# Optimization experiments

Hardware: AMD Instinct MI355X
Metric: run time of the kernel (lower is better)

## Reference

```python
import jax, jax.numpy as jnp
import numpy as np

B, N = 128, 65536
POS_FRAC = 0.02  # sparse positives, realistic for detection


def setup_inputs() -> dict:
    key = jax.random.key(0)
    k1, k2 = jax.random.split(key)
    pred = jax.random.normal(k1, (B, N), dtype=jnp.float32)
    label = (jax.random.uniform(k2, (B, N)) < POS_FRAC).astype(jnp.float32)
    return {"pred": pred, "label": label}


def _focal_loss_with_mask(pred, label, gamma=2.0, alpha=0.75, negative_ratio=3.0):
    # BCE with logits, elementwise: y*softplus(-x) + (1-y)*softplus(x)
    loss = label * jax.nn.softplus(-pred) + (1.0 - label) * jax.nn.softplus(pred)
    p = jax.nn.sigmoid(pred)
    p_t = label * p + (1.0 - label) * (1.0 - p)
    loss = loss * (1.0 - p_t) ** gamma
    loss = loss * (label * alpha + (1.0 - label) * (1.0 - alpha))

    fn_mask = (p < 0.5) & (label == 1.0)
    fp_mask = (p >= 0.5) & (label == 0.0)

    # --- hard negative mining (vectorized rank-based selection) ---
    pos_mask = label > 0
    num_pos = pos_mask.sum(axis=1, keepdims=True)              # [B,1]
    num_neg = jnp.floor(negative_ratio * num_pos).astype(jnp.int32)  # int() truncation as in torch
    loss_m = jnp.where(pos_mask, -jnp.inf, loss)               # positives sorted last
    order = jnp.argsort(-loss_m, axis=1)                       # descending sort indices
    ranks = jnp.argsort(order, axis=1)                         # rank of each element
    neg_mask = ranks < num_neg
    relevant = pos_mask | neg_mask

    w = alpha / (1.0 - alpha)
    loss = jnp.where(fn_mask | fp_mask, loss * w, loss)
    rm = relevant.astype(loss.dtype)
    return (loss * rm).sum() / rm.sum()


def reference(pred, label):
    return _focal_loss_with_mask(pred, label)
```

## Files before the change

kernel.cpp:

```cpp
#include <hip/hip_runtime.h>
#include <cstdint>
#include <cstddef>

constexpr int B_ROWS = 128;
constexpr int N_COLS = 65536;
constexpr int LIST_CAP = 8192;

constexpr size_t OFF_HISTCNT  = 0;
constexpr size_t OFF_HISTLOSS = (size_t)1 << 20;
constexpr size_t OFF_NUMPOS   = (size_t)2 << 20;
constexpr size_t OFF_SPOS     = ((size_t)2 << 20) + 512;
constexpr size_t OFF_ROWS     = ((size_t)2 << 20) + 1024;
constexpr size_t OFF_ROWDEN   = ((size_t)2 << 20) + 2048;
constexpr size_t ZERO_BYTES   = ((size_t)2 << 20) + 4096;
constexpr size_t OFF_KEYS     = (size_t)4 << 20;

__device__ __forceinline__ unsigned key_from_pred(float x) {
  unsigned b = __float_as_uint(x);
  return (b & 0x80000000u) ? ~b : (b | 0x80000000u);
}
__device__ __forceinline__ float pred_from_key(unsigned k) {
  unsigned b = (k & 0x80000000u) ? (k ^ 0x80000000u) : ~k;
  return __uint_as_float(b);
}

__device__ __forceinline__ float neg_loss(float x) {
  float ax = fabsf(x);
  float e  = expf(-ax);
  float p  = (x >= 0.0f) ? 1.0f / (1.0f + e) : e / (1.0f + e);
  float sp = fmaxf(x, 0.0f) + log1pf(e);
  float pt = 1.0f - p;
  float f  = 1.0f - pt;
  float l  = sp * f * f * 0.25f;
  return (p >= 0.5f) ? l * 3.0f : l;
}
__device__ __forceinline__ float pos_loss(float x) {
  float ax = fabsf(x);
  float e  = expf(-ax);
  float p  = (x >= 0.0f) ? 1.0f / (1.0f + e) : e / (1.0f + e);
  float sp = fmaxf(-x, 0.0f) + log1pf(e);
  float f  = 1.0f - p;
  float l  = sp * f * f * 0.75f;
  return (p < 0.5f) ? l * 3.0f : l;
}
__device__ __forceinline__ float loss_from_key(unsigned k) { return neg_loss(pred_from_key(k)); }

constexpr int K1_TPB = 256;
constexpr int K1_SEGS = 8;
constexpr int K1_SEG_ELEMS = N_COLS / K1_SEGS;
constexpr int K1_ITERS = K1_SEG_ELEMS / (K1_TPB * 4);

template <bool STORE_KEYS>
__global__ __launch_bounds__(K1_TPB)
void k1_hist(const float* __restrict__ pred, const float* __restrict__ label,
             int* __restrict__ histCnt, float* __restrict__ histLoss,
             int* __restrict__ numPos, float* __restrict__ SPos,
             unsigned* __restrict__ keys)
{
  __shared__ int   hcnt[2048];
  __shared__ float hloss[2048];
  __shared__ int   wnp[K1_TPB / 64];
  __shared__ float wsp[K1_TPB / 64];
  const int tid = threadIdx.x;
  for (int i = tid; i < 2048; i += K1_TPB) { hcnt[i] = 0; hloss[i] = 0.0f; }
  __syncthreads();

  const int row = blockIdx.x / K1_SEGS;
  const int seg = blockIdx.x % K1_SEGS;
  const size_t base = (size_t)row * N_COLS + (size_t)seg * K1_SEG_ELEMS;
  const float4* p4 = reinterpret_cast<const float4*>(pred + base);
  const float4* l4 = reinterpret_cast<const float4*>(label + base);
  uint4* k4 = STORE_KEYS ? reinterpret_cast<uint4*>(keys + base) : nullptr;

  int npos = 0; float spos = 0.0f;
  for (int it = 0; it < K1_ITERS; ++it) {
    const int vi = it * K1_TPB + tid;
    const float4 pv = p4[vi];
    const float4 lv = l4[vi];
    const float xs[4] = {pv.x, pv.y, pv.z, pv.w};
    const float ys[4] = {lv.x, lv.y, lv.z, lv.w};
    unsigned ks[4];
#pragma unroll
    for (int j = 0; j < 4; ++j) {
      const float x = xs[j];
      if (ys[j] > 0.5f) {
        npos += 1;
        spos += pos_loss(x);
        ks[j] = 0u;
      } else {
        const unsigned key = key_from_pred(x);
        ks[j] = key;
        atomicAdd(&hcnt[key >> 21], 1);
        atomicAdd(&hloss[key >> 21], neg_loss(x));
      }
    }
    if (STORE_KEYS) { uint4 uk; uk.x = ks[0]; uk.y = ks[1]; uk.z = ks[2]; uk.w = ks[3]; k4[vi] = uk; }
  }

#pragma unroll
  for (int off = 32; off > 0; off >>= 1) {
    npos += __shfl_down(npos, off);
    spos += __shfl_down(spos, off);
  }
  const int wid = tid >> 6, lane = tid & 63;
  if (lane == 0) { wnp[wid] = npos; wsp[wid] = spos; }
  __syncthreads();
  if (tid == 0) {
    int tn = 0; float ts = 0.0f;
    for (int i = 0; i < K1_TPB / 64; ++i) { tn += wnp[i]; ts += wsp[i]; }
    atomicAdd(&numPos[row], tn);
    unsafeAtomicAdd(&SPos[row], ts);
  }
  __syncthreads();
  for (int i = tid; i < 2048; i += K1_TPB) {
    if (hcnt[i]) {
      atomicAdd(&histCnt[row * 2048 + i], hcnt[i]);
      unsafeAtomicAdd(&histLoss[row * 2048 + i], hloss[i]);
    }
  }
}

constexpr int K2_TPB = 1024;

__device__ void suffix_scan(int* c, float* l, int M) {
  const int T = blockDim.x;
  const int i0 = threadIdx.x, i1 = threadIdx.x + T;
  for (int d = 1; d < M; d <<= 1) {
    int vi0 = 0, vi1 = 0; float vf0 = 0.0f, vf1 = 0.0f;
    const bool h0 = i0 < M, h1 = i1 < M;
    if (h0) { vi0 = c[i0] + ((i0 + d < M) ? c[i0 + d] : 0);
              vf0 = l[i0] + ((i0 + d < M) ? l[i0 + d] : 0.0f); }
    if (h1) { vi1 = c[i1] + ((i1 + d < M) ? c[i1 + d] : 0);
              vf1 = l[i1] + ((i1 + d < M) ? l[i1 + d] : 0.0f); }
    __syncthreads();
    if (h0) { c[i0] = vi0; l[i0] = vf0; }
    if (h1) { c[i1] = vi1; l[i1] = vf1; }
    __syncthreads();
  }
}

__device__ int find_cut(const int* sc, int M, int r, int* ctrl) {
  __syncthreads();
  if (threadIdx.x == 0) *ctrl = -1;
  __syncthreads();
  int loc = -1;
  for (int i = threadIdx.x; i < M; i += blockDim.x)
    if (sc[i] >= r) loc = i;
  if (loc >= 0) atomicMax(ctrl, loc);
  __syncthreads();
  return *ctrl;
}

template <bool USE_KEYS>
__device__ void stream_filter(const float* __restrict__ pred, const float* __restrict__ label,
                              const unsigned* __restrict__ keys, int row, int b1, int b2,
                              int* hcnt, float* hloss, unsigned* list, int* listCnt)
{
  const size_t base = (size_t)row * N_COLS;
  const int tid = threadIdx.x;

  auto handle = [&](unsigned key) {
    if ((int)(key >> 21) != b1) return;
    if (b2 < 0) {
      const int idx = atomicAdd(listCnt, 1);
      if (idx < LIST_CAP) list[idx] = key;
      const int b = (key >> 10) & 0x7FF;
      atomicAdd(&hcnt[b], 1);
      atomicAdd(&hloss[b], loss_from_key(key));
    } else {
      if ((int)((key >> 10) & 0x7FF) != b2) return;
      const int b = key & 0x3FF;
      atomicAdd(&hcnt[b], 1);
      atomicAdd(&hloss[b], loss_from_key(key));
    }
  };

  if (USE_KEYS) {
    const uint4* k4 = reinterpret_cast<const uint4*>(keys + base);
    for (int it = 0; it < N_COLS / (K2_TPB * 4); ++it) {
      const uint4 kv = k4[it * K2_TPB + tid];
      const unsigned ks[4] = {kv.x, kv.y, kv.z, kv.w};
#pragma unroll
      for (int j = 0; j < 4; ++j) {
        const unsigned key = ks[j];
        if (key == 0u) continue;
        handle(key);
      }
    }
  } else {
    const float4* p4 = reinterpret_cast<const float4*>(pred + base);
    const float4* l4 = reinterpret_cast<const float4*>(label + base);
    for (int it = 0; it < N_COLS / (K2_TPB * 4); ++it) {
      const float4 pv = p4[it * K2_TPB + tid];
      const float4 lv = l4[it * K2_TPB + tid];
      const float xs[4] = {pv.x, pv.y, pv.z, pv.w};
      const float ys[4] = {lv.x, lv.y, lv.z, lv.w};
#pragma unroll
      for (int j = 0; j < 4; ++j) {
        if (ys[j] > 0.5f) continue;
        handle(key_from_pred(xs[j]));
      }
    }
  }
}

template <bool USE_KEYS>
__global__ __launch_bounds__(K2_TPB)
void k2_select(const float* __restrict__ pred, const float* __restrict__ label,
               const unsigned* __restrict__ keys,
               const int* __restrict__ histCnt, const float* __restrict__ histLoss,
               const int* __restrict__ numPos, const float* __restrict__ SPos,
               double* __restrict__ rowS, int* __restrict__ rowDen)
{
  __shared__ int      s_cnt[2048];
  __shared__ float    s_loss[2048];
  __shared__ int      sc_cnt[1024];
  __shared__ float    sc_loss[1024];
  __shared__ unsigned s_list[LIST_CAP];
  __shared__ int      s_listCnt;
  __shared__ int      s_ctrl;

  const int tid = threadIdx.x;
  const int row = blockIdx.x;
  const int np = numPos[row];
  const int nneg = N_COLS - np;
  const int k = (3 * np < nneg) ? 3 * np : nneg;
  if (k <= 0) {
    if (tid == 0) { rowS[row] = (double)SPos[row]; rowDen[row] = np; }
    return;
  }

  for (int i = tid; i < 2048; i += K2_TPB) {
    s_cnt[i]  = histCnt[row * 2048 + i];
    s_loss[i] = histLoss[row * 2048 + i];
  }
  __syncthreads();
  suffix_scan(s_cnt, s_loss, 2048);
  const int b1 = find_cut(s_cnt, 2048, k, &s_ctrl);
  const int r1 = k - ((b1 + 1 < 2048) ? s_cnt[b1 + 1] : 0);
  float S = (b1 + 1 < 2048) ? s_loss[b1 + 1] : 0.0f;
  __syncthreads();

  for (int i = tid; i < 2048; i += K2_TPB) { s_cnt[i] = 0; s_loss[i] = 0.0f; }
  if (tid == 0) s_listCnt = 0;
  __syncthreads();
  stream_filter<USE_KEYS>(pred, label, keys, row, b1, -1, s_cnt, s_loss, s_list, &s_listCnt);
  __syncthreads();
  const int listTotal = s_listCnt;
  suffix_scan(s_cnt, s_loss, 2048);
  const int b2 = find_cut(s_cnt, 2048, r1, &s_ctrl);
  const int r2 = r1 - ((b2 + 1 < 2048) ? s_cnt[b2 + 1] : 0);
  S += (b2 + 1 < 2048) ? s_loss[b2 + 1] : 0.0f;
  __syncthreads();

  for (int i = tid; i < 1024; i += K2_TPB) { s_cnt[i] = 0; s_loss[i] = 0.0f; }
  __syncthreads();
  if (listTotal <= LIST_CAP) {
    for (int i = tid; i < listTotal; i += K2_TPB) {
      const unsigned key = s_list[i];
      if ((int)((key >> 10) & 0x7FF) == b2) {
        atomicAdd(&s_cnt[key & 0x3FF], 1);
        atomicAdd(&s_loss[key & 0x3FF], loss_from_key(key));
      }
    }
  } else {
    stream_filter<USE_KEYS>(pred, label, keys, row, b1, b2, s_cnt, s_loss, nullptr, nullptr);
  }
  __syncthreads();
  for (int i = tid; i < 1024; i += K2_TPB) { sc_cnt[i] = s_cnt[i]; sc_loss[i] = s_loss[i]; }
  __syncthreads();
  suffix_scan(sc_cnt, sc_loss, 1024);
  const int b3 = find_cut(sc_cnt, 1024, r2, &s_ctrl);
  const int r3 = r2 - ((b3 + 1 < 1024) ? sc_cnt[b3 + 1] : 0);
  S += (b3 + 1 < 1024) ? sc_loss[b3 + 1] : 0.0f;
  const float tie = s_loss[b3] / (float)s_cnt[b3];
  S += (float)r3 * tie;

  if (tid == 0) {
    rowS[row] = (double)S + (double)SPos[row];
    rowDen[row] = np + k;
  }
}

__global__ __launch_bounds__(B_ROWS)
void k3_final(const double* __restrict__ rowS, const int* __restrict__ rowDen,
              float* __restrict__ out)
{
  __shared__ double sd[B_ROWS];
  __shared__ long long si[B_ROWS];
  const int t = threadIdx.x;
  sd[t] = rowS[t];
  si[t] = (long long)rowDen[t];
  __syncthreads();
  if (t == 0) {
    double s = 0.0; long long d = 0;
    for (int i = 0; i < B_ROWS; ++i) { s += sd[i]; d += si[i]; }
    out[0] = (float)(s / (double)d);
  }
}

extern "C" void kernel_launch(void* const* d_in, const int* in_sizes, int n_in,
                              void* d_out, int out_size, void* d_ws, size_t ws_size,
                              hipStream_t stream)
{
  const float* pred  = (const float*)d_in[0];
  const float* label = (const float*)d_in[1];
  float* out = (float*)d_out;
  char* ws = (char*)d_ws;

  int*      histCnt  = (int*)(ws + OFF_HISTCNT);
  float*    histLoss = (float*)(ws + OFF_HISTLOSS);
  int*      numPos   = (int*)(ws + OFF_NUMPOS);
  float*    SPos     = (float*)(ws + OFF_SPOS);
  double*   rowS     = (double*)(ws + OFF_ROWS);
  int*      rowDen   = (int*)(ws + OFF_ROWDEN);
  unsigned* keys     = (unsigned*)(ws + OFF_KEYS);

  const bool useKeys = ws_size >= OFF_KEYS + (size_t)B_ROWS * N_COLS * sizeof(unsigned);

  hipMemsetAsync(ws, 0, ZERO_BYTES, stream);

  const dim3 g1(B_ROWS * K1_SEGS), t1(K1_TPB);
  const dim3 g2(B_ROWS), t2(K2_TPB);
  if (useKeys) {
    k1_hist<true><<<g1, t1, 0, stream>>>(pred, label, histCnt, histLoss, numPos, SPos, keys);
    k2_select<true><<<g2, t2, 0, stream>>>(pred, label, keys, histCnt, histLoss, numPos, SPos, rowS, rowDen);
  } else {
    k1_hist<false><<<g1, t1, 0, stream>>>(pred, label, histCnt, histLoss, numPos, SPos, nullptr);
    k2_select<false><<<g2, t2, 0, stream>>>(pred, label, nullptr, histCnt, histLoss, numPos, SPos, rowS, rowDen);
  }
  k3_final<<<dim3(1), dim3(B_ROWS), 0, stream>>>(rowS, rowDen, out);
}
```

Measured before the change: 213.3 us.

## Split per-row selection into cut, parallel stream-compaction, and refine kernels

The single 128-block selection kernel is split into three stages. A small kernel finds the coarse cut bin from a count-only histogram. A wide 2048-block kernel streams the keys, summing the loss of elements above the cut and compacting boundary-bin candidates into a global list with wave-ballot appends. A refine kernel then resolves the finer bins from the compacted list in shared memory. The loss histogram and its float atomics are dropped from the first pass, and the keys are streamed by many more blocks instead of one block per row. The cost is two extra launches, a candidate buffer in global memory, and a fallback rescan path when the candidates overflow the cap.

```diff
diff --git a/kernel.cpp b/kernel.cpp
--- a/kernel.cpp
+++ b/kernel.cpp
@@ -4,16 +4,23 @@
 
 constexpr int B_ROWS = 128;
 constexpr int N_COLS = 65536;
-constexpr int LIST_CAP = 8192;
-
-constexpr size_t OFF_HISTCNT  = 0;
-constexpr size_t OFF_HISTLOSS = (size_t)1 << 20;
-constexpr size_t OFF_NUMPOS   = (size_t)2 << 20;
-constexpr size_t OFF_SPOS     = ((size_t)2 << 20) + 512;
-constexpr size_t OFF_ROWS     = ((size_t)2 << 20) + 1024;
-constexpr size_t OFF_ROWDEN   = ((size_t)2 << 20) + 2048;
-constexpr size_t ZERO_BYTES   = ((size_t)2 << 20) + 4096;
-constexpr size_t OFF_KEYS     = (size_t)4 << 20;
+constexpr int CAP    = 4096;
+
+constexpr size_t OFF_HISTCNT = 0;
+constexpr size_t OFF_CAND    = (size_t)1 << 20;
+constexpr size_t OFF_MISC    = (size_t)3 << 20;
+constexpr size_t MO_NUMPOS   = 0;
+constexpr size_t MO_SPOS     = 512;
+constexpr size_t MO_ROWS     = 1024;
+constexpr size_t MO_ROWDEN   = 2048;
+constexpr size_t MO_CANDBIN  = 2560;
+constexpr size_t MO_R1       = 3072;
+constexpr size_t MO_KARR     = 3584;
+constexpr size_t MO_CANDCNT  = 4096;
+constexpr size_t MO_SABOVE   = 4608;
+constexpr size_t MO_AUTO64   = 5120;
+constexpr size_t MISC_ZERO   = 6144;
+constexpr size_t OFF_KEYS    = (size_t)4 << 20;
 
 __device__ __forceinline__ unsigned key_from_pred(float x) {
   unsigned b = __float_as_uint(x);
@@ -29,8 +36,7 @@
   float e  = expf(-ax);
   float p  = (x >= 0.0f) ? 1.0f / (1.0f + e) : e / (1.0f + e);
   float sp = fmaxf(x, 0.0f) + log1pf(e);
-  float pt = 1.0f - p;
-  float f  = 1.0f - pt;
+  float f  = p;
   float l  = sp * f * f * 0.25f;
   return (p >= 0.5f) ? l * 3.0f : l;
 }
@@ -45,6 +51,48 @@
 }
 __device__ __forceinline__ float loss_from_key(unsigned k) { return neg_loss(pred_from_key(k)); }
 
+__device__ void suffix_scan(int* c, float* l, int M) {
+  const int T = blockDim.x;
+  const int i0 = threadIdx.x, i1 = threadIdx.x + T;
+  for (int d = 1; d < M; d <<= 1) {
+    int vi0 = 0, vi1 = 0; float vf0 = 0.0f, vf1 = 0.0f;
+    const bool h0 = i0 < M, h1 = i1 < M;
+    if (h0) { vi0 = c[i0] + ((i0 + d < M) ? c[i0 + d] : 0);
+              vf0 = l[i0] + ((i0 + d < M) ? l[i0 + d] : 0.0f); }
+    if (h1) { vi1 = c[i1] + ((i1 + d < M) ? c[i1 + d] : 0);
+              vf1 = l[i1] + ((i1 + d < M) ? l[i1 + d] : 0.0f); }
+    __syncthreads();
+    if (h0) { c[i0] = vi0; l[i0] = vf0; }
+    if (h1) { c[i1] = vi1; l[i1] = vf1; }
+    __syncthreads();
+  }
+}
+__device__ void suffix_scan_i(int* c, int M) {
+  const int T = blockDim.x;
+  const int i0 = threadIdx.x, i1 = threadIdx.x + T;
+  for (int d = 1; d < M; d <<= 1) {
+    int v0 = 0, v1 = 0;
+    const bool h0 = i0 < M, h1 = i1 < M;
+    if (h0) v0 = c[i0] + ((i0 + d < M) ? c[i0 + d] : 0);
+    if (h1) v1 = c[i1] + ((i1 + d < M) ? c[i1 + d] : 0);
+    __syncthreads();
+    if (h0) c[i0] = v0;
+    if (h1) c[i1] = v1;
+    __syncthreads();
+  }
+}
+__device__ int find_cut(const int* sc, int M, int r, int* ctrl) {
+  __syncthreads();
+  if (threadIdx.x == 0) *ctrl = -1;
+  __syncthreads();
+  int loc = -1;
+  for (int i = threadIdx.x; i < M; i += blockDim.x)
+    if (sc[i] >= r) loc = i;
+  if (loc >= 0) atomicMax(ctrl, loc);
+  __syncthreads();
+  return *ctrl;
+}
+
 constexpr int K1_TPB = 256;
 constexpr int K1_SEGS = 8;
 constexpr int K1_SEG_ELEMS = N_COLS / K1_SEGS;
@@ -53,16 +101,14 @@
 template <bool STORE_KEYS>
 __global__ __launch_bounds__(K1_TPB)
 void k1_hist(const float* __restrict__ pred, const float* __restrict__ label,
-             int* __restrict__ histCnt, float* __restrict__ histLoss,
-             int* __restrict__ numPos, float* __restrict__ SPos,
+             int* __restrict__ histCnt, int* __restrict__ numPos, float* __restrict__ SPos,
              unsigned* __restrict__ keys)
 {
   __shared__ int   hcnt[2048];
-  __shared__ float hloss[2048];
   __shared__ int   wnp[K1_TPB / 64];
   __shared__ float wsp[K1_TPB / 64];
   const int tid = threadIdx.x;
-  for (int i = tid; i < 2048; i += K1_TPB) { hcnt[i] = 0; hloss[i] = 0.0f; }
+  for (int i = tid; i < 2048; i += K1_TPB) hcnt[i] = 0;
   __syncthreads();
 
   const int row = blockIdx.x / K1_SEGS;
@@ -91,7 +137,6 @@
         const unsigned key = key_from_pred(x);
         ks[j] = key;
         atomicAdd(&hcnt[key >> 21], 1);
-        atomicAdd(&hloss[key >> 21], neg_loss(x));
       }
     }
     if (STORE_KEYS) { uint4 uk; uk.x = ks[0]; uk.y = ks[1]; uk.z = ks[2]; uk.w = ks[3]; k4[vi] = uk; }
@@ -112,172 +157,232 @@
     unsafeAtomicAdd(&SPos[row], ts);
   }
   __syncthreads();
-  for (int i = tid; i < 2048; i += K1_TPB) {
-    if (hcnt[i]) {
-      atomicAdd(&histCnt[row * 2048 + i], hcnt[i]);
-      unsafeAtomicAdd(&histLoss[row * 2048 + i], hloss[i]);
-    }
-  }
-}
-
-constexpr int K2_TPB = 1024;
-
-__device__ void suffix_scan(int* c, float* l, int M) {
-  const int T = blockDim.x;
-  const int i0 = threadIdx.x, i1 = threadIdx.x + T;
-  for (int d = 1; d < M; d <<= 1) {
-    int vi0 = 0, vi1 = 0; float vf0 = 0.0f, vf1 = 0.0f;
-    const bool h0 = i0 < M, h1 = i1 < M;
-    if (h0) { vi0 = c[i0] + ((i0 + d < M) ? c[i0 + d] : 0);
-              vf0 = l[i0] + ((i0 + d < M) ? l[i0 + d] : 0.0f); }
-    if (h1) { vi1 = c[i1] + ((i1 + d < M) ? c[i1 + d] : 0);
-              vf1 = l[i1] + ((i1 + d < M) ? l[i1 + d] : 0.0f); }
-    __syncthreads();
-    if (h0) { c[i0] = vi0; l[i0] = vf0; }
-    if (h1) { c[i1] = vi1; l[i1] = vf1; }
-    __syncthreads();
-  }
-}
-
-__device__ int find_cut(const int* sc, int M, int r, int* ctrl) {
-  __syncthreads();
-  if (threadIdx.x == 0) *ctrl = -1;
-  __syncthreads();
-  int loc = -1;
-  for (int i = threadIdx.x; i < M; i += blockDim.x)
-    if (sc[i] >= r) loc = i;
-  if (loc >= 0) atomicMax(ctrl, loc);
-  __syncthreads();
-  return *ctrl;
-}
-
-template <bool USE_KEYS>
-__device__ void stream_filter(const float* __restrict__ pred, const float* __restrict__ label,
-                              const unsigned* __restrict__ keys, int row, int b1, int b2,
-                              int* hcnt, float* hloss, unsigned* list, int* listCnt)
-{
-  const size_t base = (size_t)row * N_COLS;
-  const int tid = threadIdx.x;
-
-  auto handle = [&](unsigned key) {
-    if ((int)(key >> 21) != b1) return;
-    if (b2 < 0) {
-      const int idx = atomicAdd(listCnt, 1);
-      if (idx < LIST_CAP) list[idx] = key;
-      const int b = (key >> 10) & 0x7FF;
-      atomicAdd(&hcnt[b], 1);
-      atomicAdd(&hloss[b], loss_from_key(key));
-    } else {
-      if ((int)((key >> 10) & 0x7FF) != b2) return;
-      const int b = key & 0x3FF;
-      atomicAdd(&hcnt[b], 1);
-      atomicAdd(&hloss[b], loss_from_key(key));
-    }
-  };
-
-  if (USE_KEYS) {
-    const uint4* k4 = reinterpret_cast<const uint4*>(keys + base);
-    for (int it = 0; it < N_COLS / (K2_TPB * 4); ++it) {
-      const uint4 kv = k4[it * K2_TPB + tid];
-      const unsigned ks[4] = {kv.x, kv.y, kv.z, kv.w};
-#pragma unroll
-      for (int j = 0; j < 4; ++j) {
-        const unsigned key = ks[j];
-        if (key == 0u) continue;
-        handle(key);
-      }
-    }
-  } else {
-    const float4* p4 = reinterpret_cast<const float4*>(pred + base);
-    const float4* l4 = reinterpret_cast<const float4*>(label + base);
-    for (int it = 0; it < N_COLS / (K2_TPB * 4); ++it) {
-      const float4 pv = p4[it * K2_TPB + tid];
-      const float4 lv = l4[it * K2_TPB + tid];
-      const float xs[4] = {pv.x, pv.y, pv.z, pv.w};
-      const float ys[4] = {lv.x, lv.y, lv.z, lv.w};
-#pragma unroll
-      for (int j = 0; j < 4; ++j) {
-        if (ys[j] > 0.5f) continue;
-        handle(key_from_pred(xs[j]));
-      }
-    }
-  }
-}
-
-template <bool USE_KEYS>
-__global__ __launch_bounds__(K2_TPB)
-void k2_select(const float* __restrict__ pred, const float* __restrict__ label,
-               const unsigned* __restrict__ keys,
-               const int* __restrict__ histCnt, const float* __restrict__ histLoss,
-               const int* __restrict__ numPos, const float* __restrict__ SPos,
-               double* __restrict__ rowS, int* __restrict__ rowDen)
-{
-  __shared__ int      s_cnt[2048];
-  __shared__ float    s_loss[2048];
-  __shared__ int      sc_cnt[1024];
-  __shared__ float    sc_loss[1024];
-  __shared__ unsigned s_list[LIST_CAP];
-  __shared__ int      s_listCnt;
-  __shared__ int      s_ctrl;
-
-  const int tid = threadIdx.x;
-  const int row = blockIdx.x;
+  for (int i = tid; i < 2048; i += K1_TPB)
+    if (hcnt[i]) atomicAdd(&histCnt[row * 2048 + i], hcnt[i]);
+}
+
+__global__ __launch_bounds__(1024)
+void k2a_cut(const int* __restrict__ histCnt, const int* __restrict__ numPos,
+             int* __restrict__ candBin, unsigned long long* __restrict__ auto64,
+             int* __restrict__ r1Arr, int* __restrict__ kArr)
+{
+  __shared__ int s_cnt[2048];
+  __shared__ int s_ctrl;
+  const int tid = threadIdx.x, row = blockIdx.x;
   const int np = numPos[row];
   const int nneg = N_COLS - np;
   const int k = (3 * np < nneg) ? 3 * np : nneg;
+  for (int i = tid; i < 2048; i += 1024) s_cnt[i] = histCnt[row * 2048 + i];
+  __syncthreads();
+  suffix_scan_i(s_cnt, 2048);
+  if (k <= 0) {
+    if (tid == 0) {
+      candBin[row] = -1; auto64[row] = 1ull << 32; r1Arr[row] = 0; kArr[row] = k;
+    }
+    return;
+  }
+  const int b1 = find_cut(s_cnt, 2048, k, &s_ctrl);
+  if (tid == 0) {
+    const int above = (b1 + 1 < 2048) ? s_cnt[b1 + 1] : 0;
+    candBin[row] = b1;
+    auto64[row]  = (unsigned long long)(b1 + 1) << 21;
+    r1Arr[row]   = k - above;
+    kArr[row]    = k;
+  }
+}
+
+constexpr int K2B_TPB = 256;
+constexpr int K2B_SEGS = 16;
+constexpr int K2B_SEG_ELEMS = N_COLS / K2B_SEGS;
+constexpr int K2B_ITERS = K2B_SEG_ELEMS / (K2B_TPB * 4);
+
+template <bool USE_KEYS>
+__global__ __launch_bounds__(K2B_TPB)
+void k2b_stream(const float* __restrict__ pred, const float* __restrict__ label,
+                const unsigned* __restrict__ keys,
+                const int* __restrict__ candBin, const unsigned long long* __restrict__ auto64,
+                unsigned* __restrict__ candList, int* __restrict__ candCnt,
+                float* __restrict__ S_above)
+{
+  const int tid = threadIdx.x;
+  const int row = blockIdx.x / K2B_SEGS;
+  const int seg = blockIdx.x % K2B_SEGS;
+  const size_t base = (size_t)row * N_COLS + (size_t)seg * K2B_SEG_ELEMS;
+  const int cb = candBin[row];
+  const unsigned long long at = auto64[row];
+  const int lane = tid & 63, wid = tid >> 6;
+
+  float acc = 0.0f;
+  for (int it = 0; it < K2B_ITERS; ++it) {
+    unsigned ks[4];
+    if (USE_KEYS) {
+      const uint4 kv = reinterpret_cast<const uint4*>(keys + base)[it * K2B_TPB + tid];
+      ks[0] = kv.x; ks[1] = kv.y; ks[2] = kv.z; ks[3] = kv.w;
+    } else {
+      const float4 pv = reinterpret_cast<const float4*>(pred + base)[it * K2B_TPB + tid];
+      const float4 lv = reinterpret_cast<const float4*>(label + base)[it * K2B_TPB + tid];
+      const float xs[4] = {pv.x, pv.y, pv.z, pv.w};
+      const float ys[4] = {lv.x, lv.y, lv.z, lv.w};
+#pragma unroll
+      for (int j = 0; j < 4; ++j) ks[j] = (ys[j] > 0.5f) ? 0u : key_from_pred(xs[j]);
+    }
+#pragma unroll
+    for (int j = 0; j < 4; ++j) {
+      const unsigned key = ks[j];
+      const bool isneg = key != 0u;
+      const bool autosel = isneg && ((unsigned long long)key >= at);
+      if (autosel) acc += loss_from_key(key);
+      const bool cand = isneg && !autosel && ((int)(key >> 21) == cb);
+      const unsigned long long m = __ballot(cand);
+      if (m) {
+        const int leader = __ffsll((long long)m) - 1;
+        int bidx = 0;
+        if (lane == leader) bidx = atomicAdd(&candCnt[row], (int)__popcll(m));
+        bidx = __shfl(bidx, leader, 64);
+        if (cand) {
+          const int p = (int)__popcll(m & ((1ull << lane) - 1ull));
+          const int idx = bidx + p;
+          if (idx < CAP) candList[(size_t)row * CAP + idx] = key;
+        }
+      }
+    }
+  }
+
+#pragma unroll
+  for (int off = 32; off > 0; off >>= 1) acc += __shfl_down(acc, off);
+  __shared__ float wacc[K2B_TPB / 64];
+  if (lane == 0) wacc[wid] = acc;
+  __syncthreads();
+  if (tid == 0) {
+    float t = 0.0f;
+    for (int i = 0; i < K2B_TPB / 64; ++i) t += wacc[i];
+    unsafeAtomicAdd(&S_above[row], t);
+  }
+}
+
+template <bool USE_KEYS>
+__device__ void stream_bin(const float* __restrict__ pred, const float* __restrict__ label,
+                           const unsigned* __restrict__ keys, int row, int b1, int b2,
+                           int* hcnt, float* hloss)
+{
+  const size_t base = (size_t)row * N_COLS;
+  const int tid = threadIdx.x;
+  for (int it = 0; it < N_COLS / (1024 * 4); ++it) {
+    unsigned ks[4];
+    if (USE_KEYS) {
+      const uint4 kv = reinterpret_cast<const uint4*>(keys + base)[it * 1024 + tid];
+      ks[0] = kv.x; ks[1] = kv.y; ks[2] = kv.z; ks[3] = kv.w;
+    } else {
+      const float4 pv = reinterpret_cast<const float4*>(pred + base)[it * 1024 + tid];
+      const float4 lv = reinterpret_cast<const float4*>(label + base)[it * 1024 + tid];
+      const float xs[4] = {pv.x, pv.y, pv.z, pv.w};
+      const float ys[4] = {lv.x, lv.y, lv.z, lv.w};
+#pragma unroll
+      for (int j = 0; j < 4; ++j) ks[j] = (ys[j] > 0.5f) ? 0u : key_from_pred(xs[j]);
+    }
+#pragma unroll
+    for (int j = 0; j < 4; ++j) {
+      const unsigned key = ks[j];
+      if (!key) continue;
+      if ((int)(key >> 21) != b1) continue;
+      if (b2 < 0) {
+        const int b = (key >> 10) & 0x7FF;
+        atomicAdd(&hcnt[b], 1);
+        atomicAdd(&hloss[b], loss_from_key(key));
+      } else {
+        if ((int)((key >> 10) & 0x7FF) != b2) continue;
+        const int b = key & 0x3FF;
+        atomicAdd(&hcnt[b], 1);
+        atomicAdd(&hloss[b], loss_from_key(key));
+      }
+    }
+  }
+}
+
+template <bool USE_KEYS>
+__global__ __launch_bounds__(1024)
+void k2c_refine(const float* __restrict__ pred, const float* __restrict__ label,
+                const unsigned* __restrict__ keys,
+                const int* __restrict__ numPos, const float* __restrict__ SPos,
+                const int* __restrict__ candBin, const int* __restrict__ r1Arr,
+                const int* __restrict__ kArr, const int* __restrict__ candCnt,
+                const unsigned* __restrict__ candList, const float* __restrict__ S_above,
+                double* __restrict__ rowS, int* __restrict__ rowDen)
+{
+  __shared__ unsigned s_key[CAP];
+  __shared__ float    s_lv[CAP];
+  __shared__ int      h_cnt[2048];
+  __shared__ float    h_loss[2048];
+  __shared__ int      r3cnt[1024];
+  __shared__ float    r3loss[1024];
+  __shared__ int      s_ctrl;
+
+  const int tid = threadIdx.x, row = blockIdx.x;
+  const int np = numPos[row];
+  const int k  = kArr[row];
   if (k <= 0) {
     if (tid == 0) { rowS[row] = (double)SPos[row]; rowDen[row] = np; }
     return;
   }
-
-  for (int i = tid; i < 2048; i += K2_TPB) {
-    s_cnt[i]  = histCnt[row * 2048 + i];
-    s_loss[i] = histLoss[row * 2048 + i];
-  }
-  __syncthreads();
-  suffix_scan(s_cnt, s_loss, 2048);
-  const int b1 = find_cut(s_cnt, 2048, k, &s_ctrl);
-  const int r1 = k - ((b1 + 1 < 2048) ? s_cnt[b1 + 1] : 0);
-  float S = (b1 + 1 < 2048) ? s_loss[b1 + 1] : 0.0f;
-  __syncthreads();
-
-  for (int i = tid; i < 2048; i += K2_TPB) { s_cnt[i] = 0; s_loss[i] = 0.0f; }
-  if (tid == 0) s_listCnt = 0;
-  __syncthreads();
-  stream_filter<USE_KEYS>(pred, label, keys, row, b1, -1, s_cnt, s_loss, s_list, &s_listCnt);
-  __syncthreads();
-  const int listTotal = s_listCnt;
-  suffix_scan(s_cnt, s_loss, 2048);
-  const int b2 = find_cut(s_cnt, 2048, r1, &s_ctrl);
-  const int r2 = r1 - ((b2 + 1 < 2048) ? s_cnt[b2 + 1] : 0);
-  S += (b2 + 1 < 2048) ? s_loss[b2 + 1] : 0.0f;
-  __syncthreads();
-
-  for (int i = tid; i < 1024; i += K2_TPB) { s_cnt[i] = 0; s_loss[i] = 0.0f; }
-  __syncthreads();
-  if (listTotal <= LIST_CAP) {
-    for (int i = tid; i < listTotal; i += K2_TPB) {
-      const unsigned key = s_list[i];
+  const int r1 = r1Arr[row];
+  const int b1 = candBin[row];
+  const int cc = candCnt[row];
+  float S = 0.0f;
+
+  for (int i = tid; i < 2048; i += 1024) { h_cnt[i] = 0; h_loss[i] = 0.0f; }
+  __syncthreads();
+
+  int b2, r2;
+  if (cc <= CAP) {
+    for (int i = tid; i < cc; i += 1024) {
+      const unsigned key = candList[(size_t)row * CAP + i];
+      const float l = loss_from_key(key);
+      s_key[i] = key; s_lv[i] = l;
+      const int b = (key >> 10) & 0x7FF;
+      atomicAdd(&h_cnt[b], 1);
+      atomicAdd(&h_loss[b], l);
+    }
+    __syncthreads();
+    suffix_scan(h_cnt, h_loss, 2048);
+    b2 = find_cut(h_cnt, 2048, r1, &s_ctrl);
+    r2 = r1 - ((b2 + 1 < 2048) ? h_cnt[b2 + 1] : 0);
+    S += (b2 + 1 < 2048) ? h_loss[b2 + 1] : 0.0f;
+    __syncthreads();
+
+    for (int i = tid; i < 1024; i += 1024) { r3cnt[i] = 0; r3loss[i] = 0.0f; }
+    __syncthreads();
+    for (int i = tid; i < cc; i += 1024) {
+      const unsigned key = s_key[i];
       if ((int)((key >> 10) & 0x7FF) == b2) {
-        atomicAdd(&s_cnt[key & 0x3FF], 1);
-        atomicAdd(&s_loss[key & 0x3FF], loss_from_key(key));
+        atomicAdd(&r3cnt[key & 0x3FF], 1);
+        atomicAdd(&r3loss[key & 0x3FF], s_lv[i]);
       }
     }
+    __syncthreads();
   } else {
-    stream_filter<USE_KEYS>(pred, label, keys, row, b1, b2, s_cnt, s_loss, nullptr, nullptr);
-  }
-  __syncthreads();
-  for (int i = tid; i < 1024; i += K2_TPB) { sc_cnt[i] = s_cnt[i]; sc_loss[i] = s_loss[i]; }
-  __syncthreads();
-  suffix_scan(sc_cnt, sc_loss, 1024);
-  const int b3 = find_cut(sc_cnt, 1024, r2, &s_ctrl);
-  const int r3 = r2 - ((b3 + 1 < 1024) ? sc_cnt[b3 + 1] : 0);
-  S += (b3 + 1 < 1024) ? sc_loss[b3 + 1] : 0.0f;
-  const float tie = s_loss[b3] / (float)s_cnt[b3];
-  S += (float)r3 * tie;
+    stream_bin<USE_KEYS>(pred, label, keys, row, b1, -1, h_cnt, h_loss);
+    __syncthreads();
+    suffix_scan(h_cnt, h_loss, 2048);
+    b2 = find_cut(h_cnt, 2048, r1, &s_ctrl);
+    r2 = r1 - ((b2 + 1 < 2048) ? h_cnt[b2 + 1] : 0);
+    S += (b2 + 1 < 2048) ? h_loss[b2 + 1] : 0.0f;
+    __syncthreads();
+    for (int i = tid; i < 1024; i += 1024) { r3cnt[i] = 0; r3loss[i] = 0.0f; }
+    __syncthreads();
+    stream_bin<USE_KEYS>(pred, label, keys, row, b1, b2, r3cnt, r3loss);
+    __syncthreads();
+  }
+
+  for (int i = tid; i < 1024; i += 1024) { h_cnt[i] = r3cnt[i]; h_loss[i] = r3loss[i]; }
+  __syncthreads();
+  suffix_scan(h_cnt, h_loss, 1024);
+  const int b3 = find_cut(h_cnt, 1024, r2, &s_ctrl);
+  const int r3 = r2 - ((b3 + 1 < 1024) ? h_cnt[b3 + 1] : 0);
+  S += (b3 + 1 < 1024) ? h_loss[b3 + 1] : 0.0f;
+  S += (float)r3 * (r3loss[b3] / (float)r3cnt[b3]);
 
   if (tid == 0) {
-    rowS[row] = (double)S + (double)SPos[row];
+    rowS[row] = (double)S + (double)S_above[row] + (double)SPos[row];
     rowDen[row] = np + k;
   }
 }
@@ -308,26 +413,43 @@
   float* out = (float*)d_out;
   char* ws = (char*)d_ws;
 
-  int*      histCnt  = (int*)(ws + OFF_HISTCNT);
-  float*    histLoss = (float*)(ws + OFF_HISTLOSS);
-  int*      numPos   = (int*)(ws + OFF_NUMPOS);
-  float*    SPos     = (float*)(ws + OFF_SPOS);
-  double*   rowS     = (double*)(ws + OFF_ROWS);
-  int*      rowDen   = (int*)(ws + OFF_ROWDEN);
-  unsigned* keys     = (unsigned*)(ws + OFF_KEYS);
+  int*      histCnt = (int*)(ws + OFF_HISTCNT);
+  unsigned* cand    = (unsigned*)(ws + OFF_CAND);
+  char*     misc    = ws + OFF_MISC;
+  int*      numPos  = (int*)(misc + MO_NUMPOS);
+  float*    SPos    = (float*)(misc + MO_SPOS);
+  double*   rowS    = (double*)(misc + MO_ROWS);
+  int*      rowDen  = (int*)(misc + MO_ROWDEN);
+  int*      candBin = (int*)(misc + MO_CANDBIN);
+  int*      r1Arr   = (int*)(misc + MO_R1);
+  int*      kArr    = (int*)(misc + MO_KARR);
+  int*      candCnt = (int*)(misc + MO_CANDCNT);
+  float*    S_above = (float*)(misc + MO_SABOVE);
+  unsigned long long* auto64 = (unsigned long long*)(misc + MO_AUTO64);
+  unsigned* keys    = (unsigned*)(ws + OFF_KEYS);
 
   const bool useKeys = ws_size >= OFF_KEYS + (size_t)B_ROWS * N_COLS * sizeof(unsigned);
 
-  hipMemsetAsync(ws, 0, ZERO_BYTES, stream);
+  hipMemsetAsync(ws + OFF_HISTCNT, 0, (size_t)1 << 20, stream);
+  hipMemsetAsync(ws + OFF_MISC, 0, MISC_ZERO, stream);
 
   const dim3 g1(B_ROWS * K1_SEGS), t1(K1_TPB);
-  const dim3 g2(B_ROWS), t2(K2_TPB);
+  const dim3 g2a(B_ROWS), t2a(1024);
+  const dim3 g2b(B_ROWS * K2B_SEGS), t2b(K2B_TPB);
+  const dim3 g2c(B_ROWS), t2c(1024);
+
   if (useKeys) {
-    k1_hist<true><<<g1, t1, 0, stream>>>(pred, label, histCnt, histLoss, numPos, SPos, keys);
-    k2_select<true><<<g2, t2, 0, stream>>>(pred, label, keys, histCnt, histLoss, numPos, SPos, rowS, rowDen);
+    k1_hist<true><<<g1, t1, 0, stream>>>(pred, label, histCnt, numPos, SPos, keys);
+    k2a_cut<<<g2a, t2a, 0, stream>>>(histCnt, numPos, candBin, auto64, r1Arr, kArr);
+    k2b_stream<true><<<g2b, t2b, 0, stream>>>(pred, label, keys, candBin, auto64, cand, candCnt, S_above);
+    k2c_refine<true><<<g2c, t2c, 0, stream>>>(pred, label, keys, numPos, SPos, candBin, r1Arr, kArr,
+                                              candCnt, cand, S_above, rowS, rowDen);
   } else {
-    k1_hist<false><<<g1, t1, 0, stream>>>(pred, label, histCnt, histLoss, numPos, SPos, nullptr);
-    k2_select<false><<<g2, t2, 0, stream>>>(pred, label, nullptr, histCnt, histLoss, numPos, SPos, rowS, rowDen);
+    k1_hist<false><<<g1, t1, 0, stream>>>(pred, label, histCnt, numPos, SPos, nullptr);
+    k2a_cut<<<g2a, t2a, 0, stream>>>(histCnt, numPos, candBin, auto64, r1Arr, kArr);
+    k2b_stream<false><<<g2b, t2b, 0, stream>>>(pred, label, nullptr, candBin, auto64, cand, candCnt, S_above);
+    k2c_refine<false><<<g2c, t2c, 0, stream>>>(pred, label, nullptr, numPos, SPos, candBin, r1Arr, kArr,
+                                               candCnt, cand, S_above, rowS, rowDen);
   }
   k3_final<<<dim3(1), dim3(B_ROWS), 0, stream>>>(rowS, rowDen, out);
 }
```

Result: slower. 408.1 us (+91.4%).
